# Kernel optimization log

Measured on AMD Instinct MI355X. Metric: run time of the kernel, lower is better.

## Reference

```python
import jax, jax.numpy as jnp
import numpy as np

T, N, D, L, H = 128, 256, 256, 3, 4


def _ln(x, s, b):
    m = jnp.mean(x, axis=-1, keepdims=True)
    v = jnp.mean((x - m) ** 2, axis=-1, keepdims=True)
    return (x - m) / jnp.sqrt(v + 1e-5) * s + b


def setup_inputs() -> dict:
    key = jax.random.key(0)
    ks = jax.random.split(key, 12)
    s = 0.05
    d = D
    return {
        "spatial_states": jax.random.normal(ks[0], (T, N, d), jnp.float32),
        "re_norm": jax.random.uniform(ks[1], (), jnp.float32),
        "sensor_time": jnp.cumsum(jax.random.uniform(ks[2], (T,), jnp.float32) * 0.1),
        "re_proj_w": jax.random.normal(ks[3], (d, 1), jnp.float32) * s,
        "re_proj_b": jnp.zeros((d,), jnp.float32),
        "tb_n1_s": jnp.ones((d,), jnp.float32),
        "tb_n1_b": jnp.zeros((d,), jnp.float32),
        "tb_in_w": jax.random.normal(ks[4], (3 * d, d), jnp.float32) * s,
        "tb_in_b": jnp.zeros((3 * d,), jnp.float32),
        "tb_out_w": jax.random.normal(ks[5], (d, d), jnp.float32) * s,
        "tb_out_b": jnp.zeros((d,), jnp.float32),
        "tb_n2_s": jnp.ones((d,), jnp.float32),
        "tb_n2_b": jnp.zeros((d,), jnp.float32),
        "tb_ff1_w": jax.random.normal(ks[6], (2 * d, d), jnp.float32) * s,
        "tb_ff1_b": jnp.zeros((2 * d,), jnp.float32),
        "tb_ff2_w": jax.random.normal(ks[7], (d, 2 * d), jnp.float32) * s,
        "tb_ff2_b": jnp.zeros((d,), jnp.float32),
        "cell_ff1_w": jax.random.normal(ks[8], (L, d, 2 * d), jnp.float32) * s,
        "cell_ff1_b": jnp.zeros((L, d), jnp.float32),
        "cell_ff2_w": jax.random.normal(ks[9], (L, d, 2 * d), jnp.float32) * s,
        "cell_ff2_b": jnp.zeros((L, d), jnp.float32),
        "cell_logtau": jnp.tile(jnp.linspace(-1.0, 1.0, d, dtype=jnp.float32), (L, 1)),
        "cell_tb_w": jax.random.normal(ks[10], (L, d, 2 * d), jnp.float32) * s,
        "cell_tb_b": jnp.zeros((L, d), jnp.float32),
    }


def reference(spatial_states, re_norm, sensor_time,
              re_proj_w, re_proj_b,
              tb_n1_s, tb_n1_b, tb_in_w, tb_in_b, tb_out_w, tb_out_b,
              tb_n2_s, tb_n2_b, tb_ff1_w, tb_ff1_b, tb_ff2_w, tb_ff2_b,
              cell_ff1_w, cell_ff1_b, cell_ff2_w, cell_ff2_b,
              cell_logtau, cell_tb_w, cell_tb_b):
    t, n, d = spatial_states.shape
    nL = cell_logtau.shape[0]
    hd = d // H

    # dt per step: first absolute time, then diffs (as in torch source)
    dts = jnp.concatenate([sensor_time[:1], sensor_time[1:] - sensor_time[:-1]])  # [T]
    re_bias = re_proj_w[:, 0] * re_norm + re_proj_b  # [d]

    def token_block(x):  # x: [T, N, d]; attention over N, batched over T
        y = _ln(x, tb_n1_s, tb_n1_b)
        qkv = y @ tb_in_w.T + tb_in_b
        q, k, v = jnp.split(qkv, 3, axis=-1)
        q = q.reshape(t, n, H, hd)
        k = k.reshape(t, n, H, hd)
        v = v.reshape(t, n, H, hd)
        logits = jnp.einsum('bqhd,bkhd->bhqk', q, k) / jnp.sqrt(jnp.float32(hd))
        a = jax.nn.softmax(logits, axis=-1)
        o = jnp.einsum('bhqk,bkhd->bqhd', a, v).reshape(t, n, d)
        x = x + (o @ tb_out_w.T + tb_out_b)
        y = _ln(x, tb_n2_s, tb_n2_b)
        f = jax.nn.silu(y @ tb_ff1_w.T + tb_ff1_b) @ tb_ff2_w.T + tb_ff2_b
        return x + f

    seq = spatial_states
    for l in range(nL):
        # token attention + re_bias are independent of the recurrence -> vectorize over T
        xs = token_block(seq) + re_bias  # [T, N, d]
        w1, b1 = cell_ff1_w[l], cell_ff1_b[l]
        w2, b2 = cell_ff2_w[l], cell_ff2_b[l]
        wt, bt = cell_tb_w[l], cell_tb_b[l]
        tau = jnp.exp(cell_logtau[l])  # [d]

        def step(h, xd):
            x_t, dt = xd
            xh = jnp.concatenate([x_t, h], axis=-1)  # [N, 2d]
            f1 = jnp.tanh(xh @ w1.T + b1)
            f2 = jnp.tanh(xh @ w2.T + b2)
            gate = jax.nn.sigmoid(-tau * dt + (xh @ wt.T + bt))
            h_new = gate * f1 + (1.0 - gate) * f2
            return h_new, h_new

        h0 = jnp.zeros((n, d), seq.dtype)
        _, outs = jax.lax.scan(step, h0, (xs, dts))  # outs: [T, N, d]
        seq = outs + seq if l > 0 else outs
    return seq
```

## Files before the change

### kernel.cpp

```cpp
#include <hip/hip_runtime.h>


#define T_DIM 128
#define N_DIM 256
#define D_DIM 256
#define H_DIM 4
#define HD_DIM 64
#define L_DIM 3
#define TN (T_DIM * N_DIM)

typedef __bf16 bf16x8 __attribute__((ext_vector_type(8)));
typedef __bf16 bf16x4 __attribute__((ext_vector_type(4)));
typedef float f32x4 __attribute__((ext_vector_type(4)));
typedef _Float16 f16x2 __attribute__((ext_vector_type(2)));

#define LDS_BAR()                                            \
  do {                                                       \
    asm volatile("s_waitcnt lgkmcnt(0)" ::: "memory");       \
    __builtin_amdgcn_s_barrier();                            \
    __builtin_amdgcn_sched_barrier(0);                       \
  } while (0)

__device__ inline float wave_reduce_sum(float v) {
#pragma unroll
  for (int off = 32; off > 0; off >>= 1) v += __shfl_xor(v, off);
  return v;
}

__device__ inline float bf_to_f(unsigned short u) {
  return __uint_as_float((unsigned int)u << 16);
}

__global__ __launch_bounds__(256) void ln_kernel(const float* __restrict__ x,
                                                 const float* __restrict__ sc,
                                                 const float* __restrict__ bi,
                                                 __bf16* __restrict__ y) {
  const int wid = threadIdx.x >> 6;
  const int lane = threadIdx.x & 63;
  const size_t row = (size_t)blockIdx.x * 4 + wid;
  const float4 xv = *(const float4*)(x + row * D_DIM + lane * 4);
  float s = xv.x + xv.y + xv.z + xv.w;
  float ss = xv.x * xv.x + xv.y * xv.y + xv.z * xv.z + xv.w * xv.w;
  s = wave_reduce_sum(s);
  ss = wave_reduce_sum(ss);
  const float mean = s * (1.f / D_DIM);
  const float var = ss * (1.f / D_DIM) - mean * mean;
  const float r = rsqrtf(var + 1e-5f);
  const float4 scv = *(const float4*)(sc + lane * 4);
  const float4 biv = *(const float4*)(bi + lane * 4);
  bf16x4 ov;
  ov[0] = (__bf16)((xv.x - mean) * r * scv.x + biv.x);
  ov[1] = (__bf16)((xv.y - mean) * r * scv.y + biv.y);
  ov[2] = (__bf16)((xv.z - mean) * r * scv.z + biv.z);
  ov[3] = (__bf16)((xv.w - mean) * r * scv.w + biv.w);
  *(bf16x4*)(y + row * D_DIM + lane * 4) = ov;
}

template <int EPI, int OBF>
__global__ __launch_bounds__(256) void gemm_tiled(const __bf16* __restrict__ A,
                                                  const __bf16* __restrict__ W,
                                                  const float* __restrict__ bias,
                                                  const float* __restrict__ R,
                                                  void* __restrict__ outv,
                                                  int M, int Nout, int K) {
  __shared__ __bf16 a_lds[128][72];
  __shared__ __bf16 b_lds[128][72];
  const int tid = threadIdx.x;
  const int w = tid >> 6, l = tid & 63;
  const int lr = l & 15, kg = l >> 4;
  const int wm = (w & 1) * 64, wn = (w >> 1) * 64;
  const int m0 = blockIdx.x * 128, n0 = blockIdx.y * 128;
  const int srow = tid >> 1, scol = (tid & 1) * 32;
  const __bf16* ag = A + (size_t)(m0 + srow) * K + scol;
  const __bf16* bg = W + (size_t)(n0 + srow) * K + scol;

  bf16x8 av[4], bv[4];
#pragma unroll
  for (int c = 0; c < 4; ++c) {
    av[c] = *(const bf16x8*)(ag + c * 8);
    bv[c] = *(const bf16x8*)(bg + c * 8);
  }

  f32x4 acc[4][4] = {};
  for (int k0 = 0; k0 < K; k0 += 64) {
    LDS_BAR();
#pragma unroll
    for (int c = 0; c < 4; ++c) {
      *(bf16x8*)&a_lds[srow][scol + c * 8] = av[c];
      *(bf16x8*)&b_lds[srow][scol + c * 8] = bv[c];
    }
    if (k0 + 64 < K) {
#pragma unroll
      for (int c = 0; c < 4; ++c) {
        av[c] = *(const bf16x8*)(ag + k0 + 64 + c * 8);
        bv[c] = *(const bf16x8*)(bg + k0 + 64 + c * 8);
      }
    }
    LDS_BAR();
#pragma unroll
    for (int ks = 0; ks < 2; ++ks) {
      bf16x8 af[4], bf[4];
#pragma unroll
      for (int mt = 0; mt < 4; ++mt)
        af[mt] = *(const bf16x8*)&a_lds[wm + mt * 16 + lr][ks * 32 + kg * 8];
#pragma unroll
      for (int nt = 0; nt < 4; ++nt)
        bf[nt] = *(const bf16x8*)&b_lds[wn + nt * 16 + lr][ks * 32 + kg * 8];
#pragma unroll
      for (int mt = 0; mt < 4; ++mt)
#pragma unroll
        for (int nt = 0; nt < 4; ++nt)
          acc[mt][nt] =
              __builtin_amdgcn_mfma_f32_16x16x32_bf16(af[mt], bf[nt], acc[mt][nt], 0, 0, 0);
    }
  }
#pragma unroll
  for (int nt = 0; nt < 4; ++nt) {
    const int col = n0 + wn + nt * 16 + lr;
    const float bvs = bias[col];
#pragma unroll
    for (int mt = 0; mt < 4; ++mt) {
#pragma unroll
      for (int j = 0; j < 4; ++j) {
        const int row = m0 + wm + mt * 16 + kg * 4 + j;
        float v = acc[mt][nt][j] + bvs;
        if (EPI == 1) v += R[(size_t)row * Nout + col];
        if (EPI == 2) v = v * (1.f / (1.f + __expf(-v)));
        const size_t oi = (size_t)row * Nout + col;
        if (OBF)
          ((__bf16*)outv)[oi] = (__bf16)v;
        else
          ((float*)outv)[oi] = v;
      }
    }
  }
}

__global__ __launch_bounds__(256, 2) void attn_mfma(const __bf16* __restrict__ qkv,
                                                    __bf16* __restrict__ o) {
  const int t = blockIdx.x, h = blockIdx.y;
  const int tid = threadIdx.x;
  const int w = tid >> 6, l = tid & 63;
  const int lr = l & 15, kg = l >> 4;

  __shared__ __bf16 vt_lds[64 * 256];
  __shared__ __bf16 p_lds[4][16 * 256];

  {
    const __bf16* vrow = qkv + ((size_t)(t * N_DIM + tid)) * 768 + 512 + h * HD_DIM;
#pragma unroll
    for (int c8 = 0; c8 < 64; c8 += 8) {
      bf16x8 v = *(const bf16x8*)(vrow + c8);
#pragma unroll
      for (int i = 0; i < 8; ++i) {
        const int c = c8 + i;
        const int byte = (c * 512 + tid * 2) ^ ((c & 7) << 4);
        *(__bf16*)((char*)vt_lds + byte) = v[i];
      }
    }
  }
  __syncthreads();

  const __bf16* kbase = qkv + (size_t)t * N_DIM * 768 + 256 + h * HD_DIM;
  const __bf16* qbase = qkv + (size_t)t * N_DIM * 768 + h * HD_DIM;
  char* pw = (char*)&p_lds[w][0];

  for (int qt = 0; qt < 4; ++qt) {
    const int q0 = w * 64 + qt * 16;
    const bf16x8 qf0 = *(const bf16x8*)(qbase + (size_t)(q0 + lr) * 768 + kg * 8);
    const bf16x8 qf1 = *(const bf16x8*)(qbase + (size_t)(q0 + lr) * 768 + 32 + kg * 8);
    f32x4 acc[16];
#pragma unroll
    for (int nt = 0; nt < 16; ++nt) {
      const bf16x8 a0 = *(const bf16x8*)(kbase + (size_t)(nt * 16 + lr) * 768 + kg * 8);
      const bf16x8 a1 = *(const bf16x8*)(kbase + (size_t)(nt * 16 + lr) * 768 + 32 + kg * 8);
      f32x4 s = {};
      s = __builtin_amdgcn_mfma_f32_16x16x32_bf16(a0, qf0, s, 0, 0, 0);
      s = __builtin_amdgcn_mfma_f32_16x16x32_bf16(a1, qf1, s, 0, 0, 0);
      acc[nt] = s;
    }
    float mx = -3.0e38f;
#pragma unroll
    for (int nt = 0; nt < 16; ++nt)
#pragma unroll
      for (int j = 0; j < 4; ++j) mx = fmaxf(mx, acc[nt][j]);
    mx = fmaxf(mx, __shfl_xor(mx, 16));
    mx = fmaxf(mx, __shfl_xor(mx, 32));
    float sum = 0.f;
#pragma unroll
    for (int nt = 0; nt < 16; ++nt) {
      bf16x4 pb;
#pragma unroll
      for (int j = 0; j < 4; ++j) {
        const float p = __expf((acc[nt][j] - mx) * 0.125f);
        pb[j] = (__bf16)p;
        sum += (float)pb[j];
      }
      const int byte = (lr * 512 + nt * 32 + kg * 8) ^ ((lr & 7) << 4);
      *(bf16x4*)(pw + byte) = pb;
    }
    sum += __shfl_xor(sum, 16);
    sum += __shfl_xor(sum, 32);
    const float inv = 1.f / sum;
    f32x4 oacc[4] = {};
#pragma unroll
    for (int kt = 0; kt < 8; ++kt) {
      const int pbyte = (lr * 512 + kt * 64 + kg * 16) ^ ((lr & 7) << 4);
      const bf16x8 bfrag = *(const bf16x8*)(pw + pbyte);
#pragma unroll
      for (int ct = 0; ct < 4; ++ct) {
        const int c = ct * 16 + lr;
        const int vbyte = (c * 512 + kt * 64 + kg * 16) ^ ((c & 7) << 4);
        const bf16x8 afrag = *(const bf16x8*)((char*)vt_lds + vbyte);
        oacc[ct] = __builtin_amdgcn_mfma_f32_16x16x32_bf16(afrag, bfrag, oacc[ct], 0, 0, 0);
      }
    }
    __bf16* orow = o + ((size_t)(t * N_DIM + q0 + lr)) * D_DIM + h * HD_DIM;
#pragma unroll
    for (int ct = 0; ct < 4; ++ct) {
      bf16x4 ov;
#pragma unroll
      for (int j = 0; j < 4; ++j) ov[j] = (__bf16)(oacc[ct][j] * inv);
      *(bf16x4*)(orow + ct * 16 + kg * 4) = ov;
    }
  }
}

__global__ __launch_bounds__(768, 1) void scan_dot(const __bf16* __restrict__ P,
                                                   const _Float16* __restrict__ Whf,
                                                   const float* __restrict__ logtau,
                                                   const float* __restrict__ st,
                                                   const float* __restrict__ addsrc,
                                                   float* __restrict__ out) {
  const int tid = threadIdx.x;
  const int n = blockIdx.x;
  const bool lead = tid < 256;

  __shared__ _Float16 h_buf[2][264];
  __shared__ float acc[776];
  __shared__ float dts[T_DIM];

  if (tid < T_DIM) dts[tid] = (tid == 0) ? st[0] : st[tid] - st[tid - 1];
  if (tid < 66) ((uint4*)h_buf)[tid] = (uint4){0, 0, 0, 0};

  f16x2 wr[128];
  {
    const f16x2* wp = (const f16x2*)(Whf + (size_t)tid * 256);
#pragma unroll
    for (int i = 0; i < 128; ++i) wr[i] = wp[i];
  }
  const float tau = lead ? __expf(logtau[tid]) : 0.f;

  const unsigned short* Pp = (const unsigned short*)P + (size_t)n * 768 + tid;
  float* op = out + (size_t)n * D_DIM + tid;
  const float* ap = (addsrc && lead) ? addsrc + (size_t)n * D_DIM + tid : nullptr;

  unsigned short c1 = 0, c2 = 0, c3 = 0, n1 = 0, n2 = 0, n3 = 0;
  float av = 0.f, nav = 0.f;
  if (lead) {
    c1 = Pp[0]; c2 = Pp[256]; c3 = Pp[512];
    const unsigned short* Pn = Pp + (size_t)N_DIM * 768;
    n1 = Pn[0]; n2 = Pn[256]; n3 = Pn[512];
    if (ap) {
      av = ap[0];
      nav = ap[(size_t)N_DIM * D_DIM];
    }
  }
  __syncthreads();

  for (int t = 0; t < T_DIM; ++t) {
    unsigned short m1 = 0, m2 = 0, m3 = 0;
    float mav = 0.f;
    if (lead && t + 2 < T_DIM) {
      const unsigned short* Pm = Pp + (size_t)(t + 2) * N_DIM * 768;
      m1 = Pm[0]; m2 = Pm[256]; m3 = Pm[512];
      if (ap) mav = ap[(size_t)(t + 2) * N_DIM * D_DIM];
    }

    const _Float16* hb = &h_buf[t & 1][0];
    float a = 0.f;
#pragma unroll
    for (int c = 0; c < 32; ++c) {
      const uint4 hu = *(const uint4*)(hb + c * 8);
      a = __builtin_amdgcn_fdot2(__builtin_bit_cast(f16x2, hu.x), wr[c * 4 + 0], a, false);
      a = __builtin_amdgcn_fdot2(__builtin_bit_cast(f16x2, hu.y), wr[c * 4 + 1], a, false);
      a = __builtin_amdgcn_fdot2(__builtin_bit_cast(f16x2, hu.z), wr[c * 4 + 2], a, false);
      a = __builtin_amdgcn_fdot2(__builtin_bit_cast(f16x2, hu.w), wr[c * 4 + 3], a, false);
    }
    acc[tid] = a;
    LDS_BAR();

    if (lead) {
      const float dt = dts[t];
      const float A1 = acc[tid] + bf_to_f(c1);
      const float A2 = acc[256 + tid] + bf_to_f(c2);
      const float A3 = acc[512 + tid] + bf_to_f(c3) - tau * dt;
      const float e1 = __expf(-2.f * fabsf(A1));
      const float f1 = copysignf((1.f - e1) / (1.f + e1), A1);
      const float e2 = __expf(-2.f * fabsf(A2));
      const float f2 = copysignf((1.f - e2) / (1.f + e2), A2);
      const float g = 1.f / (1.f + __expf(-A3));
      const float hn = g * f1 + (1.f - g) * f2;
      h_buf[(t + 1) & 1][tid] = (_Float16)hn;
      op[(size_t)t * N_DIM * D_DIM] = hn + av;
    }
    LDS_BAR();

    c1 = n1; c2 = n2; c3 = n3; av = nav;
    n1 = m1; n2 = m2; n3 = m3; nav = mav;
  }
}

__global__ void cvt_kernel(const float* __restrict__ src, __bf16* __restrict__ dst, int n) {
  const int i = blockIdx.x * 256 + threadIdx.x;
  if (i < n) dst[i] = (__bf16)src[i];
}

__global__ void pack_cell_kernel(const float* __restrict__ w1, const float* __restrict__ w2,
                                 const float* __restrict__ wt, __bf16* __restrict__ Wx,
                                 _Float16* __restrict__ Whf) {
  const int idx = blockIdx.x * 256 + threadIdx.x;
  if (idx >= 3 * 768 * 256) return;
  const int l = idx / (768 * 256);
  const int r2 = idx - l * (768 * 256);
  const int jj = r2 >> 8;
  const int c = r2 & 255;
  const int m = jj >> 8;
  const int r = jj & 255;
  const float* src = (m == 0 ? w1 : (m == 1 ? w2 : wt)) + ((size_t)l * 256 + r) * 512;
  Wx[(size_t)l * (768 * 256) + (size_t)jj * 256 + c] = (__bf16)src[c];
  Whf[(size_t)l * (768 * 256) + (size_t)jj * 256 + c] = (_Float16)src[256 + c];
}

__global__ void bias_pack_kernel(const float* __restrict__ b1, const float* __restrict__ b2,
                                 const float* __restrict__ bt, const float* __restrict__ ff2b,
                                 const float* __restrict__ rw, const float* __restrict__ rb,
                                 const float* __restrict__ rn, float* __restrict__ bias768,
                                 float* __restrict__ ff2bias) {
  const int idx = blockIdx.x * 256 + threadIdx.x;
  if (idx < 3 * 768) {
    const int l = idx / 768, jj = idx % 768, m = jj >> 8, r = jj & 255;
    const float* s = (m == 0 ? b1 : (m == 1 ? b2 : bt));
    bias768[idx] = s[l * 256 + r];
  }
  if (idx < 256) ff2bias[idx] = ff2b[idx] + rw[idx] * rn[0] + rb[idx];
}

extern "C" void kernel_launch(void* const* d_in, const int* in_sizes, int n_in,
                              void* d_out, int out_size, void* d_ws, size_t ws_size,
                              hipStream_t stream) {
  (void)in_sizes; (void)n_in; (void)out_size; (void)ws_size;
  const float* spatial = (const float*)d_in[0];
  const float* re_norm = (const float*)d_in[1];
  const float* sensor_time = (const float*)d_in[2];
  const float* re_proj_w = (const float*)d_in[3];
  const float* re_proj_b = (const float*)d_in[4];
  const float* n1s = (const float*)d_in[5];
  const float* n1b = (const float*)d_in[6];
  const float* in_w = (const float*)d_in[7];
  const float* in_b = (const float*)d_in[8];
  const float* out_w = (const float*)d_in[9];
  const float* out_b = (const float*)d_in[10];
  const float* n2s = (const float*)d_in[11];
  const float* n2b = (const float*)d_in[12];
  const float* ff1_w = (const float*)d_in[13];
  const float* ff1_b = (const float*)d_in[14];
  const float* ff2_w = (const float*)d_in[15];
  const float* ff2_b = (const float*)d_in[16];
  const float* c1w = (const float*)d_in[17];
  const float* c1b = (const float*)d_in[18];
  const float* c2w = (const float*)d_in[19];
  const float* c2b = (const float*)d_in[20];
  const float* clt = (const float*)d_in[21];
  const float* ctw = (const float*)d_in[22];
  const float* ctb = (const float*)d_in[23];

  char* ws = (char*)d_ws;
  size_t off = 0;
  auto alloc = [&](size_t b) {
    char* p = ws + off;
    off = (off + b + 255) & ~(size_t)255;
    return p;
  };
  float* seq = (float*)alloc((size_t)TN * D_DIM * 4);
  float* xb = (float*)alloc((size_t)TN * D_DIM * 4);
  __bf16* yb = (__bf16*)alloc((size_t)TN * D_DIM * 2);
  char* big = (char*)alloc((size_t)TN * 768 * 2);
  __bf16* qkvb = (__bf16*)big;
  __bf16* gb = (__bf16*)big;
  __bf16* Pb = (__bf16*)big;
  __bf16* w_in = (__bf16*)alloc(768 * 256 * 2);
  __bf16* w_out = (__bf16*)alloc(256 * 256 * 2);
  __bf16* w_f1 = (__bf16*)alloc(512 * 256 * 2);
  __bf16* w_f2 = (__bf16*)alloc(256 * 512 * 2);
  __bf16* Wx = (__bf16*)alloc((size_t)3 * 768 * 256 * 2);
  _Float16* Whf = (_Float16*)alloc((size_t)3 * 768 * 256 * 2);
  float* b768 = (float*)alloc(3 * 768 * 4);
  float* f2bias = (float*)alloc(256 * 4);

  cvt_kernel<<<(768 * 256 + 255) / 256, 256, 0, stream>>>(in_w, w_in, 768 * 256);
  cvt_kernel<<<(256 * 256 + 255) / 256, 256, 0, stream>>>(out_w, w_out, 256 * 256);
  cvt_kernel<<<(512 * 256 + 255) / 256, 256, 0, stream>>>(ff1_w, w_f1, 512 * 256);
  cvt_kernel<<<(256 * 512 + 255) / 256, 256, 0, stream>>>(ff2_w, w_f2, 256 * 512);
  pack_cell_kernel<<<(3 * 768 * 256 + 255) / 256, 256, 0, stream>>>(c1w, c2w, ctw, Wx, Whf);
  bias_pack_kernel<<<9, 256, 0, stream>>>(c1b, c2b, ctb, ff2_b, re_proj_w, re_proj_b,
                                          re_norm, b768, f2bias);

  for (int l = 0; l < L_DIM; ++l) {
    const float* seq_in = (l == 0) ? spatial : seq;
    ln_kernel<<<TN / 4, 256, 0, stream>>>(seq_in, n1s, n1b, yb);
    gemm_tiled<0, 1><<<dim3(TN / 128, 768 / 128), 256, 0, stream>>>(yb, w_in, in_b, nullptr,
                                                                    qkvb, TN, 768, 256);
    attn_mfma<<<dim3(T_DIM, H_DIM), 256, 0, stream>>>(qkvb, yb);
    gemm_tiled<1, 0><<<dim3(TN / 128, 256 / 128), 256, 0, stream>>>(yb, w_out, out_b, seq_in,
                                                                    xb, TN, 256, 256);
    ln_kernel<<<TN / 4, 256, 0, stream>>>(xb, n2s, n2b, yb);
    gemm_tiled<2, 1><<<dim3(TN / 128, 512 / 128), 256, 0, stream>>>(yb, w_f1, ff1_b, nullptr,
                                                                    gb, TN, 512, 256);
    gemm_tiled<1, 1><<<dim3(TN / 128, 256 / 128), 256, 0, stream>>>(gb, w_f2, f2bias, xb, yb,
                                                                    TN, 256, 512);
    gemm_tiled<0, 1><<<dim3(TN / 128, 768 / 128), 256, 0, stream>>>(
        yb, Wx + (size_t)l * 768 * 256, b768 + l * 768, nullptr, Pb, TN, 768, 256);
    float* outp = (l == 2) ? (float*)d_out : seq;
    const float* addp = (l == 0) ? nullptr : seq;
    scan_dot<<<N_DIM, 768, 0, stream>>>(Pb, Whf + (size_t)l * 768 * 256, clt + l * 256,
                                        sensor_time, addp, outp);
  }
}
```

Before: 1.117 ms.

## Store residual streams in bf16 and load GEMM weights directly from global

Switches the intermediate residual buffers (seq, xb) from fp32 to bf16, templating the layernorm, GEMM residual epilogue and scan kernels on input and output type, so less memory traffic goes through those passes. Separately, the tiled GEMM drops the LDS staging of the weight tile and reads B fragments straight from global memory (relying on cache reuse), which frees LDS and removes the B store pass. The cost is lower precision in the residual path and possibly more global/L2 traffic with uncoalesced B-fragment loads.

```diff
diff --git a/kernel.cpp b/kernel.cpp
--- a/kernel.cpp
+++ b/kernel.cpp
@@ -31,16 +31,25 @@
   return __uint_as_float((unsigned int)u << 16);
 }
 
-__global__ __launch_bounds__(256) void ln_kernel(const float* __restrict__ x,
+template <typename TI>
+__global__ __launch_bounds__(256) void ln_kernel(const TI* __restrict__ x,
                                                  const float* __restrict__ sc,
                                                  const float* __restrict__ bi,
                                                  __bf16* __restrict__ y) {
   const int wid = threadIdx.x >> 6;
   const int lane = threadIdx.x & 63;
   const size_t row = (size_t)blockIdx.x * 4 + wid;
-  const float4 xv = *(const float4*)(x + row * D_DIM + lane * 4);
-  float s = xv.x + xv.y + xv.z + xv.w;
-  float ss = xv.x * xv.x + xv.y * xv.y + xv.z * xv.z + xv.w * xv.w;
+  float xv[4];
+  if constexpr (__is_same(TI, float)) {
+    const float4 v = *(const float4*)(x + row * D_DIM + lane * 4);
+    xv[0] = v.x; xv[1] = v.y; xv[2] = v.z; xv[3] = v.w;
+  } else {
+    const bf16x4 v = *(const bf16x4*)(x + row * D_DIM + lane * 4);
+#pragma unroll
+    for (int i = 0; i < 4; ++i) xv[i] = (float)v[i];
+  }
+  float s = xv[0] + xv[1] + xv[2] + xv[3];
+  float ss = xv[0] * xv[0] + xv[1] * xv[1] + xv[2] * xv[2] + xv[3] * xv[3];
   s = wave_reduce_sum(s);
   ss = wave_reduce_sum(ss);
   const float mean = s * (1.f / D_DIM);
@@ -49,22 +58,21 @@
   const float4 scv = *(const float4*)(sc + lane * 4);
   const float4 biv = *(const float4*)(bi + lane * 4);
   bf16x4 ov;
-  ov[0] = (__bf16)((xv.x - mean) * r * scv.x + biv.x);
-  ov[1] = (__bf16)((xv.y - mean) * r * scv.y + biv.y);
-  ov[2] = (__bf16)((xv.z - mean) * r * scv.z + biv.z);
-  ov[3] = (__bf16)((xv.w - mean) * r * scv.w + biv.w);
+  ov[0] = (__bf16)((xv[0] - mean) * r * scv.x + biv.x);
+  ov[1] = (__bf16)((xv[1] - mean) * r * scv.y + biv.y);
+  ov[2] = (__bf16)((xv[2] - mean) * r * scv.z + biv.z);
+  ov[3] = (__bf16)((xv[3] - mean) * r * scv.w + biv.w);
   *(bf16x4*)(y + row * D_DIM + lane * 4) = ov;
 }
 
-template <int EPI, int OBF>
+template <int EPI, int OBF, int RBF>
 __global__ __launch_bounds__(256) void gemm_tiled(const __bf16* __restrict__ A,
                                                   const __bf16* __restrict__ W,
                                                   const float* __restrict__ bias,
-                                                  const float* __restrict__ R,
+                                                  const void* __restrict__ R,
                                                   void* __restrict__ outv,
                                                   int M, int Nout, int K) {
   __shared__ __bf16 a_lds[128][72];
-  __shared__ __bf16 b_lds[128][72];
   const int tid = threadIdx.x;
   const int w = tid >> 6, l = tid & 63;
   const int lr = l & 15, kg = l >> 4;
@@ -72,29 +80,19 @@
   const int m0 = blockIdx.x * 128, n0 = blockIdx.y * 128;
   const int srow = tid >> 1, scol = (tid & 1) * 32;
   const __bf16* ag = A + (size_t)(m0 + srow) * K + scol;
-  const __bf16* bg = W + (size_t)(n0 + srow) * K + scol;
-
-  bf16x8 av[4], bv[4];
-#pragma unroll
-  for (int c = 0; c < 4; ++c) {
-    av[c] = *(const bf16x8*)(ag + c * 8);
-    bv[c] = *(const bf16x8*)(bg + c * 8);
-  }
+
+  bf16x8 av[4];
+#pragma unroll
+  for (int c = 0; c < 4; ++c) av[c] = *(const bf16x8*)(ag + c * 8);
 
   f32x4 acc[4][4] = {};
   for (int k0 = 0; k0 < K; k0 += 64) {
     LDS_BAR();
 #pragma unroll
-    for (int c = 0; c < 4; ++c) {
-      *(bf16x8*)&a_lds[srow][scol + c * 8] = av[c];
-      *(bf16x8*)&b_lds[srow][scol + c * 8] = bv[c];
-    }
+    for (int c = 0; c < 4; ++c) *(bf16x8*)&a_lds[srow][scol + c * 8] = av[c];
     if (k0 + 64 < K) {
 #pragma unroll
-      for (int c = 0; c < 4; ++c) {
-        av[c] = *(const bf16x8*)(ag + k0 + 64 + c * 8);
-        bv[c] = *(const bf16x8*)(bg + k0 + 64 + c * 8);
-      }
+      for (int c = 0; c < 4; ++c) av[c] = *(const bf16x8*)(ag + k0 + 64 + c * 8);
     }
     LDS_BAR();
 #pragma unroll
@@ -105,7 +103,8 @@
         af[mt] = *(const bf16x8*)&a_lds[wm + mt * 16 + lr][ks * 32 + kg * 8];
 #pragma unroll
       for (int nt = 0; nt < 4; ++nt)
-        bf[nt] = *(const bf16x8*)&b_lds[wn + nt * 16 + lr][ks * 32 + kg * 8];
+        bf[nt] = *(const bf16x8*)(W + (size_t)(n0 + wn + nt * 16 + lr) * K + k0 + ks * 32 +
+                                  kg * 8);
 #pragma unroll
       for (int mt = 0; mt < 4; ++mt)
 #pragma unroll
@@ -124,9 +123,10 @@
       for (int j = 0; j < 4; ++j) {
         const int row = m0 + wm + mt * 16 + kg * 4 + j;
         float v = acc[mt][nt][j] + bvs;
-        if (EPI == 1) v += R[(size_t)row * Nout + col];
+        const size_t oi = (size_t)row * Nout + col;
+        if (EPI == 1)
+          v += RBF ? bf_to_f(((const unsigned short*)R)[oi]) : ((const float*)R)[oi];
         if (EPI == 2) v = v * (1.f / (1.f + __expf(-v)));
-        const size_t oi = (size_t)row * Nout + col;
         if (OBF)
           ((__bf16*)outv)[oi] = (__bf16)v;
         else
@@ -226,12 +226,13 @@
   }
 }
 
+template <int OUTF32>
 __global__ __launch_bounds__(768, 1) void scan_dot(const __bf16* __restrict__ P,
                                                    const _Float16* __restrict__ Whf,
                                                    const float* __restrict__ logtau,
                                                    const float* __restrict__ st,
-                                                   const float* __restrict__ addsrc,
-                                                   float* __restrict__ out) {
+                                                   const __bf16* __restrict__ addsrc,
+                                                   void* __restrict__ out) {
   const int tid = threadIdx.x;
   const int n = blockIdx.x;
   const bool lead = tid < 256;
@@ -252,11 +253,12 @@
   const float tau = lead ? __expf(logtau[tid]) : 0.f;
 
   const unsigned short* Pp = (const unsigned short*)P + (size_t)n * 768 + tid;
-  float* op = out + (size_t)n * D_DIM + tid;
-  const float* ap = (addsrc && lead) ? addsrc + (size_t)n * D_DIM + tid : nullptr;
+  const size_t obase = (size_t)n * D_DIM + tid;
+  const unsigned short* ap =
+      (addsrc && lead) ? (const unsigned short*)addsrc + obase : nullptr;
 
   unsigned short c1 = 0, c2 = 0, c3 = 0, n1 = 0, n2 = 0, n3 = 0;
-  float av = 0.f, nav = 0.f;
+  unsigned short av = 0, nav = 0;
   if (lead) {
     c1 = Pp[0]; c2 = Pp[256]; c3 = Pp[512];
     const unsigned short* Pn = Pp + (size_t)N_DIM * 768;
@@ -269,8 +271,7 @@
   __syncthreads();
 
   for (int t = 0; t < T_DIM; ++t) {
-    unsigned short m1 = 0, m2 = 0, m3 = 0;
-    float mav = 0.f;
+    unsigned short m1 = 0, m2 = 0, m3 = 0, mav = 0;
     if (lead && t + 2 < T_DIM) {
       const unsigned short* Pm = Pp + (size_t)(t + 2) * N_DIM * 768;
       m1 = Pm[0]; m2 = Pm[256]; m3 = Pm[512];
@@ -302,7 +303,12 @@
       const float g = 1.f / (1.f + __expf(-A3));
       const float hn = g * f1 + (1.f - g) * f2;
       h_buf[(t + 1) & 1][tid] = (_Float16)hn;
-      op[(size_t)t * N_DIM * D_DIM] = hn + av;
+      const float ov = hn + (ap ? bf_to_f(av) : 0.f);
+      const size_t oi = obase + (size_t)t * N_DIM * D_DIM;
+      if (OUTF32)
+        ((float*)out)[oi] = ov;
+      else
+        ((__bf16*)out)[oi] = (__bf16)ov;
     }
     LDS_BAR();
 
@@ -382,8 +388,8 @@
     off = (off + b + 255) & ~(size_t)255;
     return p;
   };
-  float* seq = (float*)alloc((size_t)TN * D_DIM * 4);
-  float* xb = (float*)alloc((size_t)TN * D_DIM * 4);
+  __bf16* seq = (__bf16*)alloc((size_t)TN * D_DIM * 2);
+  __bf16* xb = (__bf16*)alloc((size_t)TN * D_DIM * 2);
   __bf16* yb = (__bf16*)alloc((size_t)TN * D_DIM * 2);
   char* big = (char*)alloc((size_t)TN * 768 * 2);
   __bf16* qkvb = (__bf16*)big;
@@ -407,23 +413,32 @@
                                           re_norm, b768, f2bias);
 
   for (int l = 0; l < L_DIM; ++l) {
-    const float* seq_in = (l == 0) ? spatial : seq;
-    ln_kernel<<<TN / 4, 256, 0, stream>>>(seq_in, n1s, n1b, yb);
-    gemm_tiled<0, 1><<<dim3(TN / 128, 768 / 128), 256, 0, stream>>>(yb, w_in, in_b, nullptr,
-                                                                    qkvb, TN, 768, 256);
+    if (l == 0)
+      ln_kernel<float><<<TN / 4, 256, 0, stream>>>(spatial, n1s, n1b, yb);
+    else
+      ln_kernel<__bf16><<<TN / 4, 256, 0, stream>>>(seq, n1s, n1b, yb);
+    gemm_tiled<0, 1, 0><<<dim3(TN / 128, 768 / 128), 256, 0, stream>>>(
+        yb, w_in, in_b, nullptr, qkvb, TN, 768, 256);
     attn_mfma<<<dim3(T_DIM, H_DIM), 256, 0, stream>>>(qkvb, yb);
-    gemm_tiled<1, 0><<<dim3(TN / 128, 256 / 128), 256, 0, stream>>>(yb, w_out, out_b, seq_in,
-                                                                    xb, TN, 256, 256);
-    ln_kernel<<<TN / 4, 256, 0, stream>>>(xb, n2s, n2b, yb);
-    gemm_tiled<2, 1><<<dim3(TN / 128, 512 / 128), 256, 0, stream>>>(yb, w_f1, ff1_b, nullptr,
-                                                                    gb, TN, 512, 256);
-    gemm_tiled<1, 1><<<dim3(TN / 128, 256 / 128), 256, 0, stream>>>(gb, w_f2, f2bias, xb, yb,
-                                                                    TN, 256, 512);
-    gemm_tiled<0, 1><<<dim3(TN / 128, 768 / 128), 256, 0, stream>>>(
+    if (l == 0)
+      gemm_tiled<1, 1, 0><<<dim3(TN / 128, 256 / 128), 256, 0, stream>>>(
+          yb, w_out, out_b, spatial, xb, TN, 256, 256);
+    else
+      gemm_tiled<1, 1, 1><<<dim3(TN / 128, 256 / 128), 256, 0, stream>>>(
+          yb, w_out, out_b, seq, xb, TN, 256, 256);
+    ln_kernel<__bf16><<<TN / 4, 256, 0, stream>>>(xb, n2s, n2b, yb);
+    gemm_tiled<2, 1, 0><<<dim3(TN / 128, 512 / 128), 256, 0, stream>>>(
+        yb, w_f1, ff1_b, nullptr, gb, TN, 512, 256);
+    gemm_tiled<1, 1, 1><<<dim3(TN / 128, 256 / 128), 256, 0, stream>>>(
+        gb, w_f2, f2bias, xb, yb, TN, 256, 512);
+    gemm_tiled<0, 1, 0><<<dim3(TN / 128, 768 / 128), 256, 0, stream>>>(
         yb, Wx + (size_t)l * 768 * 256, b768 + l * 768, nullptr, Pb, TN, 768, 256);
-    float* outp = (l == 2) ? (float*)d_out : seq;
-    const float* addp = (l == 0) ? nullptr : seq;
-    scan_dot<<<N_DIM, 768, 0, stream>>>(Pb, Whf + (size_t)l * 768 * 256, clt + l * 256,
-                                        sensor_time, addp, outp);
-  }
-}
+    const __bf16* addp = (l == 0) ? nullptr : seq;
+    if (l == 2)
+      scan_dot<1><<<N_DIM, 768, 0, stream>>>(Pb, Whf + (size_t)l * 768 * 256,
+                                             clt + l * 256, sensor_time, addp, d_out);
+    else
+      scan_dot<0><<<N_DIM, 768, 0, stream>>>(Pb, Whf + (size_t)l * 768 * 256,
+                                             clt + l * 256, sensor_time, addp, seq);
+  }
+}
```

After: 1.233 ms. 1.1x slower.
